# Performance work log

Measured on AMD Instinct MI355X. Metric: run time of the kernel, lower is better.

Reference implementation:

```python
import jax, jax.numpy as jnp
import numpy as np

B, C, K, T = 8, 256, 64, 1000
NORM_EPS = 1e-12


def setup_inputs() -> dict:
    key = jax.random.key(0)
    k_x, k_codes, k_scales = jax.random.split(key, 3)
    init_val = 1.0 / (K * C) ** 0.5
    x = jax.random.normal(k_x, (B, C, T), dtype=jnp.float32)
    codes = jax.random.uniform(k_codes, (C, K), dtype=jnp.float32,
                               minval=-init_val, maxval=init_val)
    scales = jax.random.uniform(k_scales, (K,), dtype=jnp.float32,
                                minval=0.0, maxval=1.0)
    return {"x": x, "codes": codes, "scales": scales}


def l2_normalize(t, axis, eps=NORM_EPS):
    n = jnp.sqrt(jnp.sum(t * t, axis=axis, keepdims=True))
    n = jnp.maximum(n, eps)
    return t / n


def reference(x, codes, scales):
    # x: (B, C, T); codes: (C, K); scales: (K,)
    residual = x[:, :, None, :] - codes[None, :, :, None]      # (B, C, K, T)
    residual_l2sqr = jnp.sum(residual * residual, axis=1)      # (B, K, T)
    weights_tc = jax.nn.softmax(-scales[None, :, None] * residual_l2sqr, axis=1)  # softmax over codes K
    embeddings = jnp.einsum('bckt,bkt->bkc', residual, weights_tc) / x.shape[-1]  # (B, K, C)
    embeddings = l2_normalize(embeddings, axis=-1)
    return embeddings
```

## Files before the change

### kernel.cpp

```cpp
#include <hip/hip_runtime.h>
#include <stdint.h>

constexpr int Bn  = 8;
constexpr int Cn  = 256;
constexpr int Kn  = 64;
constexpr int Tn  = 1000;
constexpr int CH  = 32;
constexpr int NCH = 32;

constexpr int XC_P = 40;
constexpr int XT_P = 264;
constexpr int WA_P = 40;
constexpr int MW_P = 36;

typedef float f32x4 __attribute__((ext_vector_type(4)));
typedef __bf16 bf16x8 __attribute__((ext_vector_type(8)));

__device__ __forceinline__ unsigned short f2bf(float f) {
    unsigned u = __float_as_uint(f);
    return (unsigned short)((u + 0x7FFFu + ((u >> 16) & 1u)) >> 16);
}

__global__ __launch_bounds__(256) void lde_prep(
    const float* __restrict__ codes, unsigned short* __restrict__ cT,
    float* __restrict__ csq)
{
    const int k = blockIdx.x, c = threadIdx.x;
    const int lane = c & 63, wv = c >> 6;
    float v = codes[c * Kn + k];
    cT[k * Cn + c] = f2bf(v);
    float q = v * v;
#pragma unroll
    for (int off = 32; off >= 1; off >>= 1) q += __shfl_xor(q, off, 64);
    __shared__ float red[4];
    if (lane == 0) red[wv] = q;
    __syncthreads();
    if (c == 0) csq[k] = red[0] + red[1] + red[2] + red[3];
}

union SmemU {
    unsigned short xT[CH * XT_P];
    unsigned short wa[Kn * WA_P];
};

__global__ __launch_bounds__(512) void lde_ab(
    const float* __restrict__ x,
    const unsigned short* __restrict__ cT,
    const float* __restrict__ csq_g,
    const float* __restrict__ scales,
    float* __restrict__ part,
    float* __restrict__ Sp)
{
    __shared__ __align__(16) unsigned short xc[Cn * XC_P];
    __shared__ __align__(16) SmemU u;
    __shared__ float Mw[Kn * MW_P];
    __shared__ float xsqp[16 * 33];
    __shared__ float xsq[CH];
    __shared__ float spw[8 * 64];

    const int tid  = threadIdx.x;
    const int wave = tid >> 6;
    const int lane = tid & 63;
    const int b    = blockIdx.x >> 5;
    const int ch   = blockIdx.x & 31;
    const int t0   = ch * CH;
    const int n    = lane & 15;
    const int q    = lane >> 4;
    const float* xb = x + (size_t)b * Cn * Tn;

#pragma unroll
    for (int r = 0; r < 4; ++r) {
        int idx = r * 512 + tid;
        int c = idx >> 3, qq = idx & 7;
        int t = t0 + 4 * qq;
        float4 v;
        if (t + 3 < Tn) {
            v = *(const float4*)(xb + c * Tn + t);
        } else {
            v.x = (t     < Tn) ? xb[c * Tn + t]     : 0.f;
            v.y = (t + 1 < Tn) ? xb[c * Tn + t + 1] : 0.f;
            v.z = (t + 2 < Tn) ? xb[c * Tn + t + 2] : 0.f;
            v.w = (t + 3 < Tn) ? xb[c * Tn + t + 3] : 0.f;
        }
        *(ushort4*)(xc + c * XC_P + 4 * qq) =
            make_ushort4(f2bf(v.x), f2bf(v.y), f2bf(v.z), f2bf(v.w));
    }

    {
        int tl = tid & 31, s = tid >> 5;
        float a = 0.f;
        if (t0 + tl < Tn) {
            const float* xp = xb + (s * 16) * Tn + t0 + tl;
#pragma unroll
            for (int i = 0; i < 16; ++i) {
                float v = xp[i * Tn];
                a = fmaf(v, v, a);
            }
        }
        xsqp[s * 33 + tl] = a;
    }
    __syncthreads();

#pragma unroll
    for (int r = 0; r < 2; ++r) {
        int idx = r * 512 + tid;
        int t = idx & 31, cg = idx >> 5;
        unsigned short tmp[8];
#pragma unroll
        for (int i = 0; i < 8; ++i) tmp[i] = xc[(cg * 8 + i) * XC_P + t];
        *(ushort4*)(u.xT + t * XT_P + cg * 8)     = make_ushort4(tmp[0], tmp[1], tmp[2], tmp[3]);
        *(ushort4*)(u.xT + t * XT_P + cg * 8 + 4) = make_ushort4(tmp[4], tmp[5], tmp[6], tmp[7]);
    }
    if (tid < CH) {
        float a = 0.f;
#pragma unroll
        for (int s = 0; s < 16; ++s) a += xsqp[s * 33 + tid];
        xsq[tid] = a;
    }
    __syncthreads();

    {
        const int kt = wave & 3, tt = wave >> 2;
        const int k = kt * 16 + n;
        const int t = tt * 16 + n;
        f32x4 acc = {0.f, 0.f, 0.f, 0.f};
        const unsigned short* Ab = cT + k * Cn + q * 8;
        const unsigned short* Bb = u.xT + t * XT_P + q * 8;
#pragma unroll
        for (int c0 = 0; c0 < Cn; c0 += 32) {
            bf16x8 aF = *(const bf16x8*)(Ab + c0);
            bf16x8 bF = *(const bf16x8*)(Bb + c0);
            acc = __builtin_amdgcn_mfma_f32_16x16x32_bf16(aF, bF, acc, 0, 0, 0);
        }
#pragma unroll
        for (int r = 0; r < 4; ++r)
            Mw[(kt * 16 + q * 4 + r) * MW_P + tt * 16 + n] = acc[r];
    }
    __syncthreads();

    {
        const float sc = scales[lane];
        const float cq = csq_g[lane];
        unsigned short wh[4];
        float sp = 0.f;
#pragma unroll
        for (int j = 0; j < 4; ++j) {
            int t = wave * 4 + j;
            float m     = Mw[lane * MW_P + t];
            float logit = -sc * (xsq[t] - 2.f * m + cq);
            float mx = logit;
#pragma unroll
            for (int off = 32; off >= 1; off >>= 1)
                mx = fmaxf(mx, __shfl_xor(mx, off, 64));
            float e = __expf(logit - mx);
            float s = e;
#pragma unroll
            for (int off = 32; off >= 1; off >>= 1)
                s += __shfl_xor(s, off, 64);
            float wv = e / s;
            if (t0 + t >= Tn) wv = 0.f;
            sp += wv;
            wh[j] = f2bf(wv);
        }
        *(ushort4*)(u.wa + lane * WA_P + wave * 4) =
            make_ushort4(wh[0], wh[1], wh[2], wh[3]);
        spw[wave * 64 + lane] = sp;
    }
    __syncthreads();

    if (wave == 0) {
        float s8 = 0.f;
#pragma unroll
        for (int w = 0; w < 8; ++w) s8 += spw[w * 64 + lane];
        Sp[((size_t)b * Kn + lane) * NCH + ch] = s8;
    }
    {
        const int kt = wave & 3, hf = wave >> 2;
        bf16x8 aF = *(const bf16x8*)(u.wa + (kt * 16 + n) * WA_P + q * 8);
#pragma unroll
        for (int i = 0; i < 8; ++i) {
            int c0 = (hf * 8 + i) * 16;
            bf16x8 bF = *(const bf16x8*)(xc + (c0 + n) * XC_P + q * 8);
            f32x4 acc = {0.f, 0.f, 0.f, 0.f};
            acc = __builtin_amdgcn_mfma_f32_16x16x32_bf16(aF, bF, acc, 0, 0, 0);
            float* pb = part + ((size_t)(b * Kn + kt * 16 + q * 4) * NCH + ch) * Cn + c0 + n;
#pragma unroll
            for (int r = 0; r < 4; ++r)
                pb[(size_t)r * NCH * Cn] = acc[r];
        }
    }
}

__global__ __launch_bounds__(256) void lde_finish(
    const float* __restrict__ part,
    const float* __restrict__ Sp,
    const float* __restrict__ codes,
    float* __restrict__ out)
{
    const int b    = blockIdx.x >> 6;
    const int k    = blockIdx.x & 63;
    const int tid  = threadIdx.x;
    const int lane = tid & 63;
    const int wave = tid >> 6;

    __shared__ float red[4];

    float s = Sp[((size_t)b * Kn + k) * NCH + (tid & 31)];
#pragma unroll
    for (int off = 16; off >= 1; off >>= 1) s += __shfl_xor(s, off, 64);

    const int c = tid;
    const float* pb = part + ((size_t)b * Kn + k) * NCH * Cn + c;
    float val = 0.f;
#pragma unroll
    for (int chk = 0; chk < NCH; ++chk) val += pb[chk * Cn];

    float e = (val - codes[c * Kn + k] * s) * (1.0f / (float)Tn);

    float qq = e * e;
#pragma unroll
    for (int off = 32; off >= 1; off >>= 1) qq += __shfl_xor(qq, off, 64);
    if (lane == 0) red[wave] = qq;
    __syncthreads();
    float nn = sqrtf(red[0] + red[1] + red[2] + red[3]);

    out[((size_t)b * Kn + k) * Cn + c] = e / fmaxf(nn, 1e-12f);
}

extern "C" void kernel_launch(void* const* d_in, const int* in_sizes, int n_in,
                              void* d_out, int out_size, void* d_ws, size_t ws_size,
                              hipStream_t stream) {
    const float* x      = (const float*)d_in[0];
    const float* codes  = (const float*)d_in[1];
    const float* scales = (const float*)d_in[2];
    float* out = (float*)d_out;

    float* part = (float*)d_ws;
    float* Sp   = part + (size_t)Bn * Kn * NCH * Cn;
    float* csq  = Sp + (size_t)Bn * Kn * NCH;
    unsigned short* cT = (unsigned short*)(csq + 64);

    lde_prep  <<<Kn,       256, 0, stream>>>(codes, cT, csq);
    lde_ab    <<<Bn * NCH, 512, 0, stream>>>(x, cT, csq, scales, part, Sp);
    lde_finish<<<Bn * Kn,  256, 0, stream>>>(part, Sp, codes, out);
}
```

Baseline: 78.06 us.

## Split assignment and pooling into separate kernels with coarser time partials

The fused assign+pool kernel becomes two kernels. The first computes the softmax weights over 16-timestep chunks and writes them as bf16 to global memory. The second re-reads x tiled by 16 channels by 256 timesteps and computes pooled partials over 4 time quarters instead of 32 chunks. This greatly shrinks the partial-sum buffer the finish kernel must read and removes the in-shared-memory transpose. The cost is an extra kernel launch, a second read of x, and a global round trip for the weights.

```diff
diff --git a/kernel.cpp b/kernel.cpp
--- a/kernel.cpp
+++ b/kernel.cpp
@@ -5,13 +5,14 @@
 constexpr int Cn  = 256;
 constexpr int Kn  = 64;
 constexpr int Tn  = 1000;
-constexpr int CH  = 32;
-constexpr int NCH = 32;
-
-constexpr int XC_P = 40;
+constexpr int CH  = 16;
+constexpr int NCH = 64;
+constexpr int TW  = 256;
+constexpr int NTQ = 4;
+
 constexpr int XT_P = 264;
-constexpr int WA_P = 40;
-constexpr int MW_P = 36;
+constexpr int MW_P = 20;
+constexpr int XC_P = 264;
 
 typedef float f32x4 __attribute__((ext_vector_type(4)));
 typedef __bf16 bf16x8 __attribute__((ext_vector_type(8)));
@@ -38,41 +39,35 @@
     if (c == 0) csq[k] = red[0] + red[1] + red[2] + red[3];
 }
 
-union SmemU {
-    unsigned short xT[CH * XT_P];
-    unsigned short wa[Kn * WA_P];
-};
-
-__global__ __launch_bounds__(512) void lde_ab(
+__global__ __launch_bounds__(256) void lde_w(
     const float* __restrict__ x,
     const unsigned short* __restrict__ cT,
     const float* __restrict__ csq_g,
     const float* __restrict__ scales,
-    float* __restrict__ part,
+    unsigned short* __restrict__ w_g,
     float* __restrict__ Sp)
 {
-    __shared__ __align__(16) unsigned short xc[Cn * XC_P];
-    __shared__ __align__(16) SmemU u;
+    __shared__ __align__(16) unsigned short xT[CH * XT_P];
     __shared__ float Mw[Kn * MW_P];
-    __shared__ float xsqp[16 * 33];
+    __shared__ float xsqp[16 * 17];
     __shared__ float xsq[CH];
-    __shared__ float spw[8 * 64];
+    __shared__ float spw[4 * 64];
 
     const int tid  = threadIdx.x;
     const int wave = tid >> 6;
     const int lane = tid & 63;
-    const int b    = blockIdx.x >> 5;
-    const int ch   = blockIdx.x & 31;
-    const int t0   = ch * CH;
     const int n    = lane & 15;
     const int q    = lane >> 4;
+    const int b    = blockIdx.x >> 6;
+    const int ch   = blockIdx.x & 63;
+    const int t0   = ch * CH;
     const float* xb = x + (size_t)b * Cn * Tn;
 
 #pragma unroll
     for (int r = 0; r < 4; ++r) {
-        int idx = r * 512 + tid;
-        int c = idx >> 3, qq = idx & 7;
-        int t = t0 + 4 * qq;
+        int idx = r * 256 + tid;
+        int c = idx >> 2, tf = idx & 3;
+        int t = t0 + 4 * tf;
         float4 v;
         if (t + 3 < Tn) {
             v = *(const float4*)(xb + c * Tn + t);
@@ -82,50 +77,34 @@
             v.z = (t + 2 < Tn) ? xb[c * Tn + t + 2] : 0.f;
             v.w = (t + 3 < Tn) ? xb[c * Tn + t + 3] : 0.f;
         }
-        *(ushort4*)(xc + c * XC_P + 4 * qq) =
-            make_ushort4(f2bf(v.x), f2bf(v.y), f2bf(v.z), f2bf(v.w));
-    }
-
+        xT[(4 * tf + 0) * XT_P + c] = f2bf(v.x);
+        xT[(4 * tf + 1) * XT_P + c] = f2bf(v.y);
+        xT[(4 * tf + 2) * XT_P + c] = f2bf(v.z);
+        xT[(4 * tf + 3) * XT_P + c] = f2bf(v.w);
+    }
     {
-        int tl = tid & 31, s = tid >> 5;
+        int tl = tid & 15, s = tid >> 4;
         float a = 0.f;
         if (t0 + tl < Tn) {
             const float* xp = xb + (s * 16) * Tn + t0 + tl;
 #pragma unroll
-            for (int i = 0; i < 16; ++i) {
-                float v = xp[i * Tn];
-                a = fmaf(v, v, a);
-            }
-        }
-        xsqp[s * 33 + tl] = a;
-    }
-    __syncthreads();
-
-#pragma unroll
-    for (int r = 0; r < 2; ++r) {
-        int idx = r * 512 + tid;
-        int t = idx & 31, cg = idx >> 5;
-        unsigned short tmp[8];
-#pragma unroll
-        for (int i = 0; i < 8; ++i) tmp[i] = xc[(cg * 8 + i) * XC_P + t];
-        *(ushort4*)(u.xT + t * XT_P + cg * 8)     = make_ushort4(tmp[0], tmp[1], tmp[2], tmp[3]);
-        *(ushort4*)(u.xT + t * XT_P + cg * 8 + 4) = make_ushort4(tmp[4], tmp[5], tmp[6], tmp[7]);
-    }
+            for (int i = 0; i < 16; ++i) { float v = xp[i * Tn]; a = fmaf(v, v, a); }
+        }
+        xsqp[s * 17 + tl] = a;
+    }
+    __syncthreads();
+
     if (tid < CH) {
         float a = 0.f;
 #pragma unroll
-        for (int s = 0; s < 16; ++s) a += xsqp[s * 33 + tid];
+        for (int s = 0; s < 16; ++s) a += xsqp[s * 17 + tid];
         xsq[tid] = a;
     }
-    __syncthreads();
 
     {
-        const int kt = wave & 3, tt = wave >> 2;
-        const int k = kt * 16 + n;
-        const int t = tt * 16 + n;
+        const unsigned short* Ab = cT + (wave * 16 + n) * Cn + q * 8;
+        const unsigned short* Bb = xT + n * XT_P + q * 8;
         f32x4 acc = {0.f, 0.f, 0.f, 0.f};
-        const unsigned short* Ab = cT + k * Cn + q * 8;
-        const unsigned short* Bb = u.xT + t * XT_P + q * 8;
 #pragma unroll
         for (int c0 = 0; c0 < Cn; c0 += 32) {
             bf16x8 aF = *(const bf16x8*)(Ab + c0);
@@ -134,7 +113,7 @@
         }
 #pragma unroll
         for (int r = 0; r < 4; ++r)
-            Mw[(kt * 16 + q * 4 + r) * MW_P + tt * 16 + n] = acc[r];
+            Mw[(wave * 16 + q * 4 + r) * MW_P + n] = acc[r];
     }
     __syncthreads();
 
@@ -162,36 +141,74 @@
             sp += wv;
             wh[j] = f2bf(wv);
         }
-        *(ushort4*)(u.wa + lane * WA_P + wave * 4) =
+        *(ushort4*)(w_g + ((size_t)(b * NCH + ch) * Kn + lane) * CH + wave * 4) =
             make_ushort4(wh[0], wh[1], wh[2], wh[3]);
         spw[wave * 64 + lane] = sp;
     }
     __syncthreads();
 
     if (wave == 0) {
-        float s8 = 0.f;
-#pragma unroll
-        for (int w = 0; w < 8; ++w) s8 += spw[w * 64 + lane];
-        Sp[((size_t)b * Kn + lane) * NCH + ch] = s8;
-    }
-    {
-        const int kt = wave & 3, hf = wave >> 2;
-        bf16x8 aF = *(const bf16x8*)(u.wa + (kt * 16 + n) * WA_P + q * 8);
-#pragma unroll
-        for (int i = 0; i < 8; ++i) {
-            int c0 = (hf * 8 + i) * 16;
-            bf16x8 bF = *(const bf16x8*)(xc + (c0 + n) * XC_P + q * 8);
-            f32x4 acc = {0.f, 0.f, 0.f, 0.f};
-            acc = __builtin_amdgcn_mfma_f32_16x16x32_bf16(aF, bF, acc, 0, 0, 0);
-            float* pb = part + ((size_t)(b * Kn + kt * 16 + q * 4) * NCH + ch) * Cn + c0 + n;
-#pragma unroll
-            for (int r = 0; r < 4; ++r)
-                pb[(size_t)r * NCH * Cn] = acc[r];
-        }
-    }
-}
-
-__global__ __launch_bounds__(256) void lde_finish(
+        float s4 = spw[lane] + spw[64 + lane] + spw[128 + lane] + spw[192 + lane];
+        Sp[((size_t)b * Kn + lane) * NCH + ch] = s4;
+    }
+}
+
+__global__ __launch_bounds__(256) void lde_pool(
+    const float* __restrict__ x,
+    const unsigned short* __restrict__ w_g,
+    float* __restrict__ part)
+{
+    __shared__ __align__(16) unsigned short xc[16 * XC_P];
+
+    const int tid  = threadIdx.x;
+    const int wave = tid >> 6;
+    const int lane = tid & 63;
+    const int n    = lane & 15;
+    const int q    = lane >> 4;
+    const int bid  = blockIdx.x;
+    const int b    = bid >> 6;
+    const int ct   = (bid >> 2) & 15;
+    const int tq   = bid & 3;
+    const int c0   = ct * 16;
+    const int tw0  = tq * TW;
+    const float* xb = x + (size_t)(b * Cn + c0) * Tn;
+
+#pragma unroll
+    for (int r = 0; r < 4; ++r) {
+        int idx = r * 256 + tid;
+        int cl = idx >> 6, tf = idx & 63;
+        int t = tw0 + 4 * tf;
+        float4 v;
+        if (t + 3 < Tn) {
+            v = *(const float4*)(xb + cl * Tn + t);
+        } else {
+            v.x = (t     < Tn) ? xb[cl * Tn + t]     : 0.f;
+            v.y = (t + 1 < Tn) ? xb[cl * Tn + t + 1] : 0.f;
+            v.z = (t + 2 < Tn) ? xb[cl * Tn + t + 2] : 0.f;
+            v.w = (t + 3 < Tn) ? xb[cl * Tn + t + 3] : 0.f;
+        }
+        *(ushort4*)(xc + cl * XC_P + 4 * tf) =
+            make_ushort4(f2bf(v.x), f2bf(v.y), f2bf(v.z), f2bf(v.w));
+    }
+    __syncthreads();
+
+    f32x4 acc = {0.f, 0.f, 0.f, 0.f};
+#pragma unroll
+    for (int s = 0; s < 8; ++s) {
+        int tg  = tw0 + s * 32 + q * 8;
+        int chh = tg >> 4;
+        int tl  = tg & 15;
+        bf16x8 aF = *(const bf16x8*)(w_g + ((size_t)(b * NCH + chh) * Kn + wave * 16 + n) * CH + tl);
+        bf16x8 bF = *(const bf16x8*)(xc + n * XC_P + s * 32 + q * 8);
+        acc = __builtin_amdgcn_mfma_f32_16x16x32_bf16(aF, bF, acc, 0, 0, 0);
+    }
+    float* pb = part + ((size_t)(b * NTQ + tq) * Kn + wave * 16 + q * 4) * Cn + c0 + n;
+#pragma unroll
+    for (int r = 0; r < 4; ++r)
+        pb[(size_t)r * Cn] = acc[r];
+}
+
+__global__ __launch_bounds__(256) void lde_fin(
     const float* __restrict__ part,
     const float* __restrict__ Sp,
     const float* __restrict__ codes,
@@ -204,18 +221,22 @@
     const int wave = tid >> 6;
 
     __shared__ float red[4];
-
-    float s = Sp[((size_t)b * Kn + k) * NCH + (tid & 31)];
-#pragma unroll
-    for (int off = 16; off >= 1; off >>= 1) s += __shfl_xor(s, off, 64);
+    __shared__ float Ss;
+
+    if (wave == 0) {
+        float s = Sp[((size_t)b * Kn + k) * NCH + lane];
+#pragma unroll
+        for (int off = 32; off >= 1; off >>= 1) s += __shfl_xor(s, off, 64);
+        if (lane == 0) Ss = s;
+    }
+    __syncthreads();
+    const float S = Ss;
 
     const int c = tid;
-    const float* pb = part + ((size_t)b * Kn + k) * NCH * Cn + c;
-    float val = 0.f;
-#pragma unroll
-    for (int chk = 0; chk < NCH; ++chk) val += pb[chk * Cn];
-
-    float e = (val - codes[c * Kn + k] * s) * (1.0f / (float)Tn);
+    const float* pb = part + (size_t)b * NTQ * Kn * Cn + k * Cn + c;
+    float val = pb[0] + pb[(size_t)Kn * Cn] + pb[(size_t)2 * Kn * Cn] + pb[(size_t)3 * Kn * Cn];
+
+    float e = (val - codes[c * Kn + k] * S) * (1.0f / (float)Tn);
 
     float qq = e * e;
 #pragma unroll
@@ -235,12 +256,15 @@
     const float* scales = (const float*)d_in[2];
     float* out = (float*)d_out;
 
-    float* part = (float*)d_ws;
-    float* Sp   = part + (size_t)Bn * Kn * NCH * Cn;
-    float* csq  = Sp + (size_t)Bn * Kn * NCH;
-    unsigned short* cT = (unsigned short*)(csq + 64);
-
-    lde_prep  <<<Kn,       256, 0, stream>>>(codes, cT, csq);
-    lde_ab    <<<Bn * NCH, 512, 0, stream>>>(x, cT, csq, scales, part, Sp);
-    lde_finish<<<Bn * Kn,  256, 0, stream>>>(part, Sp, codes, out);
-}
+    char* ws = (char*)d_ws;
+    float*          part = (float*)ws;
+    unsigned short* w_g  = (unsigned short*)(ws + (2u << 20));
+    float*          Sp   = (float*)(ws + (3u << 20));
+    unsigned short* cT   = (unsigned short*)(ws + (3u << 20) + (256u << 10));
+    float*          csq  = (float*)(ws + (3u << 20) + (292u << 10));
+
+    lde_prep<<<Kn,            256, 0, stream>>>(codes, cT, csq);
+    lde_w   <<<Bn * NCH,      256, 0, stream>>>(x, cT, csq, scales, w_g, Sp);
+    lde_pool<<<Bn * 16 * NTQ, 256, 0, stream>>>(x, w_g, part);
+    lde_fin <<<Bn * Kn,       256, 0, stream>>>(part, Sp, codes, out);
+}
```

After: 77.63 us. No clear change (-0.6%).
